# Kernel tuning notes

Hardware: AMD Instinct MI355X
Metric: run time of the kernel (lower is better)

The kernel has to match this reference:

```python
import jax, jax.numpy as jnp
import numpy as np

N_HEAD = 8
N_FEAT = 512
D_HEAD = N_FEAT // N_HEAD


def setup_inputs() -> dict:
    key = jax.random.key(0)
    ks = jax.random.split(key, 11)
    B, T, L = 4, 2048, 16
    s = 1.0 / np.sqrt(D_HEAD)
    so = 1.0 / np.sqrt(N_FEAT)
    return {
        "q": jax.random.normal(ks[0], (B, T, 1, N_FEAT), jnp.float32),
        "k": jax.random.normal(ks[1], (B, T, L, N_FEAT), jnp.float32),
        "v": jax.random.normal(ks[2], (B, T, L, N_FEAT), jnp.float32),
        "Wq": jax.random.uniform(ks[3], (D_HEAD, D_HEAD), jnp.float32, -s, s),
        "bq": jax.random.uniform(ks[4], (D_HEAD,), jnp.float32, -s, s),
        "Wk": jax.random.uniform(ks[5], (D_HEAD, D_HEAD), jnp.float32, -s, s),
        "bk": jax.random.uniform(ks[6], (D_HEAD,), jnp.float32, -s, s),
        "Wv": jax.random.uniform(ks[7], (D_HEAD, D_HEAD), jnp.float32, -s, s),
        "bv": jax.random.uniform(ks[8], (D_HEAD,), jnp.float32, -s, s),
        "Wo": jax.random.uniform(ks[9], (N_FEAT, N_FEAT), jnp.float32, -so, so),
        "bo": jax.random.uniform(ks[10], (N_FEAT,), jnp.float32, -so, so),
    }


def reference(q, k, v, Wq, bq, Wk, bk, Wv, bv, Wo, bo):
    B, T, L, F = k.shape
    H, D = N_HEAD, D_HEAD
    # split heads: q [B,T,H,D] (query axis of length 1 squeezed), k/v [B,T,L,H,D]
    qh = q.reshape(B, T, H, D)
    kh = k.reshape(B, T, L, H, D)
    vh = v.reshape(B, T, L, H, D)
    # per-head linear projections (shared across heads), Linear: x @ W^T + b
    qh = jnp.einsum("bthd,ed->bthe", qh, Wq) + bq
    kh = jnp.einsum("btlhd,ed->btlhe", kh, Wk) + bk
    vh = jnp.einsum("btlhd,ed->btlhe", vh, Wv) + bv
    # attention scores over the local window L (query length 1 per timestep)
    attw = jnp.einsum("bthd,btlhd->bthl", qh, kh) / jnp.sqrt(jnp.asarray(D, qh.dtype))
    attn = jax.nn.softmax(attw, axis=-1)  # dropout is identity in eval mode
    ct = jnp.einsum("bthl,btlhd->bthd", attn, vh)
    ct = ct.reshape(B, T, F)
    return ct @ Wo.T + bo
```

## Files before the change

kernel.cpp:

```cpp
#include <hip/hip_runtime.h>


#define NFEAT 512
#define NHEAD 8
#define DHEAD 64
#define LWIN  16
#define WPOS  8
#define NBT   32

typedef __attribute__((ext_vector_type(8))) short bf16x8;
typedef __attribute__((ext_vector_type(4))) float f32x4;

__device__ __forceinline__ unsigned short f2bf(float f) {
    unsigned int u = __float_as_uint(f);
    unsigned int r = (u + 0x7fffu + ((u >> 16) & 1u)) >> 16;
    return (unsigned short)r;
}

__device__ __forceinline__ void gload16(const float* src, float* dst) {
    __builtin_amdgcn_global_load_lds((const __attribute__((address_space(1))) float*)src,
                                     (__attribute__((address_space(3))) float*)dst,
                                     16, 0, 0);
}

__global__ void precompute_small(const float* __restrict__ Wq, const float* __restrict__ bq,
                                 const float* __restrict__ Wk,
                                 const float* __restrict__ Wo, const float* __restrict__ bo,
                                 const float* __restrict__ bv,
                                 float* __restrict__ A, float* __restrict__ g,
                                 float* __restrict__ b2) {
    int idx = blockIdx.x * 256 + threadIdx.x;
    if (idx < 4096) {
        int d = idx >> 6, dp = idx & 63;
        float s = 0.f;
        #pragma unroll 8
        for (int e = 0; e < 64; ++e) s = fmaf(Wq[e * 64 + d], Wk[e * 64 + dp], s);
        A[idx] = s;
    } else if (idx < 4160) {
        int dp = idx - 4096;
        float s = 0.f;
        #pragma unroll 8
        for (int e = 0; e < 64; ++e) s = fmaf(Wk[e * 64 + dp], bq[e], s);
        g[dp] = s;
    } else if (idx < 4672) {
        int j = idx - 4160;
        float s = bo[j];
        #pragma unroll 8
        for (int i = 0; i < 512; ++i) s = fmaf(Wo[j * 512 + i], bv[i & 63], s);
        b2[j] = s;
    }
}

__global__ void precompute_wo2(const float* __restrict__ Wo, const float* __restrict__ Wv,
                               unsigned short* __restrict__ Wo2B) {
    int idx = blockIdx.x * 256 + threadIdx.x;
    int i = idx & 511, j = idx >> 9;
    int h = i >> 6, e = i & 63;
    float s = 0.f;
    #pragma unroll 8
    for (int d = 0; d < 64; ++d)
        s = fmaf(Wo[j * 512 + h * 64 + d], Wv[d * 64 + e], s);
    Wo2B[(size_t)j * 512 + i] = f2bf(s);
}

__global__ __launch_bounds__(512, 4)
void w_prepass(const float* __restrict__ q, const float* __restrict__ A,
               const float* __restrict__ g, float* __restrict__ Wm) {
    __shared__ float As[4096];
    __shared__ float qs[WPOS][NFEAT];
    const int tid = threadIdx.x;
    const int bt0 = blockIdx.x * WPOS;

    #pragma unroll
    for (int i = 0; i < 8; ++i) As[i * 512 + tid] = A[i * 512 + tid];
    #pragma unroll
    for (int r = 0; r < WPOS; ++r) qs[r][tid] = q[(size_t)(bt0 + r) * NFEAT + tid];
    __syncthreads();

    const int e  = tid & 63;
    const int hb = (tid >> 6) << 6;
    float acc[WPOS];
    const float ge = g[e];
    #pragma unroll
    for (int r = 0; r < WPOS; ++r) acc[r] = ge;

    #pragma unroll 4
    for (int dq = 0; dq < 16; ++dq) {
        const float a0 = As[(4 * dq + 0) * 64 + e];
        const float a1 = As[(4 * dq + 1) * 64 + e];
        const float a2 = As[(4 * dq + 2) * 64 + e];
        const float a3 = As[(4 * dq + 3) * 64 + e];
        #pragma unroll
        for (int r = 0; r < WPOS; ++r) {
            const float4 qv = *reinterpret_cast<const float4*>(&qs[r][hb + 4 * dq]);
            acc[r] = fmaf(qv.x, a0, acc[r]);
            acc[r] = fmaf(qv.y, a1, acc[r]);
            acc[r] = fmaf(qv.z, a2, acc[r]);
            acc[r] = fmaf(qv.w, a3, acc[r]);
        }
    }
    #pragma unroll
    for (int r = 0; r < WPOS; ++r)
        Wm[(size_t)(bt0 + r) * NFEAT + tid] = acc[r] * 0.125f;
}

__global__ __launch_bounds__(512, 2)
void attn_stream(const float* __restrict__ Wm, const float* __restrict__ k,
                 const float* __restrict__ v, unsigned short* __restrict__ vbarG,
                 int BT) {
    __shared__ __align__(16) float kbuf[2][LWIN][NFEAT];
    __shared__ __align__(16) float vbuf[2][LWIN][NFEAT];

    const int tid  = threadIdx.x;
    const int w    = tid >> 6;
    const int lane = tid & 63;
    const int lq   = lane >> 2;
    const int d4   = lane & 3;
    const int bt0  = blockIdx.x * NBT;

    const int wmoff = w * 64 + d4 * 16;
    float4 wmc0, wmc1, wmc2, wmc3, wmn0, wmn1, wmn2, wmn3;
    {
        const float* p = Wm + (size_t)bt0 * NFEAT + wmoff;
        wmc0 = *(const float4*)(p + 0);
        wmc1 = *(const float4*)(p + 4);
        wmc2 = *(const float4*)(p + 8);
        wmc3 = *(const float4*)(p + 12);
    }

    {
        const float* kb = k + (size_t)bt0 * (LWIN * NFEAT);
        const float* vb = v + (size_t)bt0 * (LWIN * NFEAT);
        #pragma unroll
        for (int rr = 0; rr < 2; ++rr) {
            const int r    = 2 * w + rr;
            const int kofs = ((lane * 16) ^ ((r & 7) << 4)) >> 2;
            gload16(kb + r * NFEAT +       kofs,     &kbuf[0][r][0]);
            gload16(kb + r * NFEAT + 256 + kofs,     &kbuf[0][r][256]);
            gload16(vb + r * NFEAT +       lane * 4, &vbuf[0][r][0]);
            gload16(vb + r * NFEAT + 256 + lane * 4, &vbuf[0][r][256]);
        }
    }
    __syncthreads();

    const int half  = (w >> 2) & 1;
    const int hwoff = (w & 3) * 256 + d4 * 64;
    const int swz   = (lq & 7) << 4;

    for (int i = 0; i < NBT; ++i) {
        const int cur = i & 1;
        const int bt  = bt0 + i;

        if (i + 1 < NBT) {
            const float* kb = k + (size_t)(bt + 1) * (LWIN * NFEAT);
            const float* vb = v + (size_t)(bt + 1) * (LWIN * NFEAT);
            const int nb = cur ^ 1;
            #pragma unroll
            for (int rr = 0; rr < 2; ++rr) {
                const int r    = 2 * w + rr;
                const int kofs = ((lane * 16) ^ ((r & 7) << 4)) >> 2;
                gload16(kb + r * NFEAT +       kofs,     &kbuf[nb][r][0]);
                gload16(kb + r * NFEAT + 256 + kofs,     &kbuf[nb][r][256]);
                gload16(vb + r * NFEAT +       lane * 4, &vbuf[nb][r][0]);
                gload16(vb + r * NFEAT + 256 + lane * 4, &vbuf[nb][r][256]);
            }
        }
        {
            const int btn = (i + 1 < NBT) ? bt + 1 : bt;
            const float* p = Wm + (size_t)btn * NFEAT + wmoff;
            wmn0 = *(const float4*)(p + 0);
            wmn1 = *(const float4*)(p + 4);
            wmn2 = *(const float4*)(p + 8);
            wmn3 = *(const float4*)(p + 12);
        }
        __builtin_amdgcn_sched_barrier(0);

        const char* rowb = (const char*)&kbuf[cur][lq][0] + half * 1024;
        const float4 k0 = *(const float4*)(rowb + ((hwoff +  0) ^ swz));
        const float4 k1 = *(const float4*)(rowb + ((hwoff + 16) ^ swz));
        const float4 k2 = *(const float4*)(rowb + ((hwoff + 32) ^ swz));
        const float4 k3 = *(const float4*)(rowb + ((hwoff + 48) ^ swz));
        float s0 = wmc0.x * k0.x, s1 = wmc1.x * k1.x, s2 = wmc2.x * k2.x, s3 = wmc3.x * k3.x;
        s0 = fmaf(wmc0.y, k0.y, s0); s1 = fmaf(wmc1.y, k1.y, s1);
        s2 = fmaf(wmc2.y, k2.y, s2); s3 = fmaf(wmc3.y, k3.y, s3);
        s0 = fmaf(wmc0.z, k0.z, s0); s1 = fmaf(wmc1.z, k1.z, s1);
        s2 = fmaf(wmc2.z, k2.z, s2); s3 = fmaf(wmc3.z, k3.z, s3);
        s0 = fmaf(wmc0.w, k0.w, s0); s1 = fmaf(wmc1.w, k1.w, s1);
        s2 = fmaf(wmc2.w, k2.w, s2); s3 = fmaf(wmc3.w, k3.w, s3);
        float s = (s0 + s1) + (s2 + s3);
        s += __shfl_xor(s, 1, 64);
        s += __shfl_xor(s, 2, 64);
        const float e = __expf(s);

        float den = 0.f, acc = 0.f;
        #pragma unroll
        for (int l = 0; l < LWIN; ++l) {
            const float el = __shfl(e, 4 * l, 64);
            den += el;
            acc = fmaf(el, vbuf[cur][l][w * 64 + lane], acc);
        }
        vbarG[(size_t)bt * NFEAT + tid] = f2bf(acc * (1.0f / den));

        wmc0 = wmn0; wmc1 = wmn1; wmc2 = wmn2; wmc3 = wmn3;
        __syncthreads();
    }
    (void)BT;
}

__global__ __launch_bounds__(512, 4)
void out_gemm(const unsigned short* __restrict__ vbarBF,
              const unsigned short* __restrict__ Wo2B,
              const float* __restrict__ b2, float* __restrict__ out) {
    const int tid  = threadIdx.x;
    const int w    = tid >> 6;
    const int lane = tid & 63;
    const int mt   = blockIdx.x;
    const int n0   = w * 64;
    const int r    = lane & 15;
    const int kg   = lane >> 4;

    const short* Ab  = (const short*)vbarBF + ((size_t)(mt * 16 + r)) * 512 + kg * 8;
    const short* Bb0 = (const short*)Wo2B + ((size_t)(n0 +  0 + r)) * 512 + kg * 8;
    const short* Bb1 = (const short*)Wo2B + ((size_t)(n0 + 16 + r)) * 512 + kg * 8;
    const short* Bb2 = (const short*)Wo2B + ((size_t)(n0 + 32 + r)) * 512 + kg * 8;
    const short* Bb3 = (const short*)Wo2B + ((size_t)(n0 + 48 + r)) * 512 + kg * 8;

    f32x4 acc0 = {0.f, 0.f, 0.f, 0.f}, acc1 = acc0, acc2 = acc0, acc3 = acc0;

    #pragma unroll 4
    for (int kk = 0; kk < 16; ++kk) {
        const bf16x8 a   = *reinterpret_cast<const bf16x8*>(Ab  + kk * 32);
        const bf16x8 b0  = *reinterpret_cast<const bf16x8*>(Bb0 + kk * 32);
        const bf16x8 b1  = *reinterpret_cast<const bf16x8*>(Bb1 + kk * 32);
        const bf16x8 b2v = *reinterpret_cast<const bf16x8*>(Bb2 + kk * 32);
        const bf16x8 b3  = *reinterpret_cast<const bf16x8*>(Bb3 + kk * 32);
        acc0 = __builtin_amdgcn_mfma_f32_16x16x32_bf16(a, b0,  acc0, 0, 0, 0);
        acc1 = __builtin_amdgcn_mfma_f32_16x16x32_bf16(a, b1,  acc1, 0, 0, 0);
        acc2 = __builtin_amdgcn_mfma_f32_16x16x32_bf16(a, b2v, acc2, 0, 0, 0);
        acc3 = __builtin_amdgcn_mfma_f32_16x16x32_bf16(a, b3,  acc3, 0, 0, 0);
    }

    const float bb0 = b2[n0 + 0 + r],  bb1 = b2[n0 + 16 + r];
    const float bb2 = b2[n0 + 32 + r], bb3 = b2[n0 + 48 + r];
    #pragma unroll
    for (int j = 0; j < 4; ++j) {
        const size_t row = (size_t)(mt * 16 + kg * 4 + j) * 512;
        out[row + n0 +  0 + r] = acc0[j] + bb0;
        out[row + n0 + 16 + r] = acc1[j] + bb1;
        out[row + n0 + 32 + r] = acc2[j] + bb2;
        out[row + n0 + 48 + r] = acc3[j] + bb3;
    }
}

extern "C" void kernel_launch(void* const* d_in, const int* in_sizes, int n_in,
                              void* d_out, int out_size, void* d_ws, size_t ws_size,
                              hipStream_t stream) {
    const float* q  = (const float*)d_in[0];
    const float* k  = (const float*)d_in[1];
    const float* v  = (const float*)d_in[2];
    const float* Wq = (const float*)d_in[3];
    const float* bq = (const float*)d_in[4];
    const float* Wk = (const float*)d_in[5];
    const float* Wv = (const float*)d_in[7];
    const float* bv = (const float*)d_in[8];
    const float* Wo = (const float*)d_in[9];
    const float* bo = (const float*)d_in[10];
    float* out = (float*)d_out;

    float* ws = (float*)d_ws;
    float*          A      = ws;
    float*          g      = ws + 4096;
    float*          b2     = ws + 4160;
    unsigned short* Wo2B   = (unsigned short*)(ws + 4672);
    float*          Wm     = ws + 4672 + 131072;
    unsigned short* vbarG  = (unsigned short*)(ws + 4672 + 131072 + 4194304);

    const int BT = in_sizes[0] / NFEAT;

    hipLaunchKernelGGL(precompute_small, dim3(19), dim3(256), 0, stream,
                       Wq, bq, Wk, Wo, bo, bv, A, g, b2);
    hipLaunchKernelGGL(precompute_wo2, dim3(1024), dim3(256), 0, stream,
                       Wo, Wv, Wo2B);
    hipLaunchKernelGGL(w_prepass, dim3(BT / WPOS), dim3(512), 0, stream,
                       q, A, g, Wm);
    hipLaunchKernelGGL(attn_stream, dim3(BT / NBT), dim3(512), 0, stream,
                       Wm, k, v, vbarG, BT);
    hipLaunchKernelGGL(out_gemm, dim3(BT / 16), dim3(512), 0, stream,
                       vbarG, Wo2B, b2, out);
}
```

Before: 211.4 us.

## Prefetch K/V/Wm tiles two steps ahead with explicit vmcnt waits in attn_stream

Restructures the attention streaming loop so each iteration issues the K/V tile two timesteps ahead. Wm is now loaded into LDS through global_load_lds instead of registers. The single __syncthreads is replaced by explicit s_waitcnt vmcnt counts and two raw s_barriers, so more loads stay in flight while the current tile is computed. Launch bounds drop to 1 block per CU, which may change occupancy and register allocation. The hard-coded vmcnt counts depend on exact instruction counts and would be fragile if the compiler reorders loads.

```diff
diff --git a/kernel.cpp b/kernel.cpp
--- a/kernel.cpp
+++ b/kernel.cpp
@@ -21,6 +21,11 @@
     __builtin_amdgcn_global_load_lds((const __attribute__((address_space(1))) float*)src,
                                      (__attribute__((address_space(3))) float*)dst,
                                      16, 0, 0);
+}
+__device__ __forceinline__ void gload4(const float* src, float* dst) {
+    __builtin_amdgcn_global_load_lds((const __attribute__((address_space(1))) float*)src,
+                                     (__attribute__((address_space(3))) float*)dst,
+                                     4, 0, 0);
 }
 
 __global__ void precompute_small(const float* __restrict__ Wq, const float* __restrict__ bq,
@@ -104,12 +109,12 @@
         Wm[(size_t)(bt0 + r) * NFEAT + tid] = acc[r] * 0.125f;
 }
 
-__global__ __launch_bounds__(512, 2)
+__global__ __launch_bounds__(512, 1)
 void attn_stream(const float* __restrict__ Wm, const float* __restrict__ k,
-                 const float* __restrict__ v, unsigned short* __restrict__ vbarG,
-                 int BT) {
+                 const float* __restrict__ v, unsigned short* __restrict__ vbarG) {
     __shared__ __align__(16) float kbuf[2][LWIN][NFEAT];
     __shared__ __align__(16) float vbuf[2][LWIN][NFEAT];
+    __shared__ __align__(16) float wmbuf[2][NFEAT];
 
     const int tid  = threadIdx.x;
     const int w    = tid >> 6;
@@ -118,30 +123,24 @@
     const int d4   = lane & 3;
     const int bt0  = blockIdx.x * NBT;
 
-    const int wmoff = w * 64 + d4 * 16;
-    float4 wmc0, wmc1, wmc2, wmc3, wmn0, wmn1, wmn2, wmn3;
-    {
-        const float* p = Wm + (size_t)bt0 * NFEAT + wmoff;
-        wmc0 = *(const float4*)(p + 0);
-        wmc1 = *(const float4*)(p + 4);
-        wmc2 = *(const float4*)(p + 8);
-        wmc3 = *(const float4*)(p + 12);
-    }
-
-    {
-        const float* kb = k + (size_t)bt0 * (LWIN * NFEAT);
-        const float* vb = v + (size_t)bt0 * (LWIN * NFEAT);
-        #pragma unroll
-        for (int rr = 0; rr < 2; ++rr) {
-            const int r    = 2 * w + rr;
-            const int kofs = ((lane * 16) ^ ((r & 7) << 4)) >> 2;
-            gload16(kb + r * NFEAT +       kofs,     &kbuf[0][r][0]);
-            gload16(kb + r * NFEAT + 256 + kofs,     &kbuf[0][r][256]);
-            gload16(vb + r * NFEAT +       lane * 4, &vbuf[0][r][0]);
-            gload16(vb + r * NFEAT + 256 + lane * 4, &vbuf[0][r][256]);
-        }
-    }
-    __syncthreads();
+    #define ISSUE_TILE(buf, bti)                                                  \
+    {                                                                             \
+        const float* kb_ = k + (size_t)(bti) * (LWIN * NFEAT);                    \
+        const float* vb_ = v + (size_t)(bti) * (LWIN * NFEAT);                    \
+        _Pragma("unroll")                                                         \
+        for (int rr = 0; rr < 2; ++rr) {                                          \
+            const int r_    = 2 * w + rr;                                         \
+            const int kofs_ = ((lane * 16) ^ ((r_ & 7) << 4)) >> 2;               \
+            gload16(kb_ + r_ * NFEAT +       kofs_,     &kbuf[buf][r_][0]);       \
+            gload16(kb_ + r_ * NFEAT + 256 + kofs_,     &kbuf[buf][r_][256]);     \
+            gload16(vb_ + r_ * NFEAT +       lane * 4,  &vbuf[buf][r_][0]);       \
+            gload16(vb_ + r_ * NFEAT + 256 + lane * 4,  &vbuf[buf][r_][256]);     \
+        }                                                                         \
+        gload4(Wm + (size_t)(bti) * NFEAT + w * 64 + lane, &wmbuf[buf][w * 64]);  \
+    }
+
+    ISSUE_TILE(0, bt0 + 0);
+    ISSUE_TILE(1, bt0 + 1);
 
     const int half  = (w >> 2) & 1;
     const int hwoff = (w & 3) * 256 + d4 * 64;
@@ -152,41 +151,32 @@
         const int bt  = bt0 + i;
 
         if (i + 1 < NBT) {
-            const float* kb = k + (size_t)(bt + 1) * (LWIN * NFEAT);
-            const float* vb = v + (size_t)(bt + 1) * (LWIN * NFEAT);
-            const int nb = cur ^ 1;
-            #pragma unroll
-            for (int rr = 0; rr < 2; ++rr) {
-                const int r    = 2 * w + rr;
-                const int kofs = ((lane * 16) ^ ((r & 7) << 4)) >> 2;
-                gload16(kb + r * NFEAT +       kofs,     &kbuf[nb][r][0]);
-                gload16(kb + r * NFEAT + 256 + kofs,     &kbuf[nb][r][256]);
-                gload16(vb + r * NFEAT +       lane * 4, &vbuf[nb][r][0]);
-                gload16(vb + r * NFEAT + 256 + lane * 4, &vbuf[nb][r][256]);
-            }
-        }
-        {
-            const int btn = (i + 1 < NBT) ? bt + 1 : bt;
-            const float* p = Wm + (size_t)btn * NFEAT + wmoff;
-            wmn0 = *(const float4*)(p + 0);
-            wmn1 = *(const float4*)(p + 4);
-            wmn2 = *(const float4*)(p + 8);
-            wmn3 = *(const float4*)(p + 12);
-        }
-        __builtin_amdgcn_sched_barrier(0);
+            asm volatile("s_waitcnt vmcnt(9)" ::: "memory");
+        } else {
+            asm volatile("s_waitcnt vmcnt(1)" ::: "memory");
+        }
+        __builtin_amdgcn_sched_barrier(0);
+        __builtin_amdgcn_s_barrier();
+        __builtin_amdgcn_sched_barrier(0);
+
+        const float* wmp = &wmbuf[cur][w * 64 + d4 * 16];
+        const float4 wm0 = *(const float4*)(wmp + 0);
+        const float4 wm1 = *(const float4*)(wmp + 4);
+        const float4 wm2 = *(const float4*)(wmp + 8);
+        const float4 wm3 = *(const float4*)(wmp + 12);
 
         const char* rowb = (const char*)&kbuf[cur][lq][0] + half * 1024;
         const float4 k0 = *(const float4*)(rowb + ((hwoff +  0) ^ swz));
         const float4 k1 = *(const float4*)(rowb + ((hwoff + 16) ^ swz));
         const float4 k2 = *(const float4*)(rowb + ((hwoff + 32) ^ swz));
         const float4 k3 = *(const float4*)(rowb + ((hwoff + 48) ^ swz));
-        float s0 = wmc0.x * k0.x, s1 = wmc1.x * k1.x, s2 = wmc2.x * k2.x, s3 = wmc3.x * k3.x;
-        s0 = fmaf(wmc0.y, k0.y, s0); s1 = fmaf(wmc1.y, k1.y, s1);
-        s2 = fmaf(wmc2.y, k2.y, s2); s3 = fmaf(wmc3.y, k3.y, s3);
-        s0 = fmaf(wmc0.z, k0.z, s0); s1 = fmaf(wmc1.z, k1.z, s1);
-        s2 = fmaf(wmc2.z, k2.z, s2); s3 = fmaf(wmc3.z, k3.z, s3);
-        s0 = fmaf(wmc0.w, k0.w, s0); s1 = fmaf(wmc1.w, k1.w, s1);
-        s2 = fmaf(wmc2.w, k2.w, s2); s3 = fmaf(wmc3.w, k3.w, s3);
+        float s0 = wm0.x * k0.x, s1 = wm1.x * k1.x, s2 = wm2.x * k2.x, s3 = wm3.x * k3.x;
+        s0 = fmaf(wm0.y, k0.y, s0); s1 = fmaf(wm1.y, k1.y, s1);
+        s2 = fmaf(wm2.y, k2.y, s2); s3 = fmaf(wm3.y, k3.y, s3);
+        s0 = fmaf(wm0.z, k0.z, s0); s1 = fmaf(wm1.z, k1.z, s1);
+        s2 = fmaf(wm2.z, k2.z, s2); s3 = fmaf(wm3.z, k3.z, s3);
+        s0 = fmaf(wm0.w, k0.w, s0); s1 = fmaf(wm1.w, k1.w, s1);
+        s2 = fmaf(wm2.w, k2.w, s2); s3 = fmaf(wm3.w, k3.w, s3);
         float s = (s0 + s1) + (s2 + s3);
         s += __shfl_xor(s, 1, 64);
         s += __shfl_xor(s, 2, 64);
@@ -201,10 +191,16 @@
         }
         vbarG[(size_t)bt * NFEAT + tid] = f2bf(acc * (1.0f / den));
 
-        wmc0 = wmn0; wmc1 = wmn1; wmc2 = wmn2; wmc3 = wmn3;
-        __syncthreads();
-    }
-    (void)BT;
+        __builtin_amdgcn_sched_barrier(0);
+        __builtin_amdgcn_s_barrier();
+        __builtin_amdgcn_sched_barrier(0);
+
+        if (i + 2 < NBT) {
+            ISSUE_TILE(cur, bt + 2);
+        }
+        __builtin_amdgcn_sched_barrier(0);
+    }
+    #undef ISSUE_TILE
 }
 
 __global__ __launch_bounds__(512, 4)
@@ -284,7 +280,7 @@
     hipLaunchKernelGGL(w_prepass, dim3(BT / WPOS), dim3(512), 0, stream,
                        q, A, g, Wm);
     hipLaunchKernelGGL(attn_stream, dim3(BT / NBT), dim3(512), 0, stream,
-                       Wm, k, v, vbarG, BT);
+                       Wm, k, v, vbarG);
     hipLaunchKernelGGL(out_gemm, dim3(BT / 16), dim3(512), 0, stream,
                        vbarG, Wo2B, b2, out);
 }
```

Result: no change. 209.8 us (-0.8%).
